# Performance work log

Hardware: AMD Instinct MI355X
Metric: run time of the kernel (lower is better)

Reference implementation:

```python
import jax, jax.numpy as jnp
import numpy as np

NNODE = 50000
NEDGE = 1600000
ZMAX = 16      # species one-hot width
DIM = 64
SUBDIM = 8
HIDDEN = 64


def setup_inputs() -> dict:
    key = jax.random.key(0)
    ks = jax.random.split(key, 16)
    species = jax.random.randint(ks[0], (NNODE,), 0, ZMAX)
    edge_src = jax.random.randint(ks[1], (NEDGE,), 0, NNODE)
    edge_dst = jax.random.randint(ks[2], (NEDGE,), 0, NNODE)
    # distances strictly positive, inside cutoff 5.0
    distances = jax.random.uniform(ks[3], (NEDGE,)) * 4.5 + 0.5
    switch = jax.random.uniform(ks[4], (NEDGE,))
    vec = jax.random.normal(ks[5], (NEDGE, 3))
    # FullyConnectedNet([64,64,64,dim]) on input of width 1 + ZMAX
    d_in = 1 + ZMAX
    def dense_init(k, fan_in, fan_out):
        return jax.random.normal(k, (fan_in, fan_out)) / np.sqrt(fan_in)
    W1 = dense_init(ks[6], d_in, HIDDEN); b1 = jnp.zeros((HIDDEN,))
    W2 = dense_init(ks[7], HIDDEN, HIDDEN); b2 = jnp.zeros((HIDDEN,))
    W3 = dense_init(ks[8], HIDDEN, HIDDEN); b3 = jnp.zeros((HIDDEN,))
    W4 = dense_init(ks[9], HIDDEN, DIM); b4 = jnp.zeros((DIM,))
    return {
        "species": species, "edge_src": edge_src, "edge_dst": edge_dst,
        "distances": distances, "switch": switch, "vec": vec,
        "W1": W1, "b1": b1, "W2": W2, "b2": b2,
        "W3": W3, "b3": b3, "W4": W4, "b4": b4,
    }


def reference(species, edge_src, edge_dst, distances, switch, vec,
              W1, b1, W2, b2, W3, b3, W4, b4):
    onehot = jax.nn.one_hot(species, ZMAX, dtype=distances.dtype)  # (N, Z)
    d = distances[:, None]                                          # (E, 1)
    sw = switch[:, None]                                            # (E, 1)
    vhat = vec / d                                                  # (E, 3)
    sij = sw / d                                                    # (E, 1), divide_distances=True
    Rij = jnp.concatenate((sij, sij * vhat), axis=-1)               # (E, 4)
    # radial_basis is None -> radial_terms = sij; concat with species onehot of dst
    x = jnp.concatenate((sij, onehot[edge_dst]), axis=-1)           # (E, 1+Z)
    h = jax.nn.silu(x @ W1 + b1)
    h = jax.nn.silu(h @ W2 + b2)
    h = jax.nn.silu(h @ W3 + b3)
    Gij = h @ W4 + b4                                               # (E, dim)
    # scatter-sum outer product over edges -> (N, 4, dim)
    GRi = jax.ops.segment_sum(Gij[:, None, :] * Rij[:, :, None], edge_src,
                              num_segments=NNODE)
    GRisub = GRi[:, :, :SUBDIM]                                     # (N, 4, subdim)
    # contract over the 4-axis: (N, dim, subdim) -> flatten
    embedding = jnp.einsum('nad,nas->nds', GRi, GRisub).reshape(NNODE, DIM * SUBDIM)
    return embedding
```

## Files before the change

### kernel.cpp

```cpp
#include <hip/hip_runtime.h>

#define NNODE 50000
#define NEDGE 1600000
#define SCAN_BLOCKS 196
#define NBLOCKS 1024
#define NWAVES (NBLOCKS*8)
#define EPW 196

typedef __attribute__((ext_vector_type(8))) _Float16 half8;
typedef __attribute__((ext_vector_type(2))) __fp16 fp16x2;
typedef __attribute__((ext_vector_type(4))) float f32x4;
typedef __attribute__((ext_vector_type(2))) float f32x2;

union H2U { fp16x2 h; unsigned int u; };
union H8U { half8 h8; unsigned int u[4]; };

__device__ __forceinline__ float b2f(unsigned short u) {
    return __uint_as_float(((unsigned int)u) << 16);
}
__device__ __forceinline__ f32x2 lo2(f32x4 v) { f32x2 r; r.x = v[0]; r.y = v[1]; return r; }
__device__ __forceinline__ f32x2 hi2(f32x4 v) { f32x2 r; r.x = v[2]; r.y = v[3]; return r; }

__device__ __forceinline__ unsigned int silu2_pk(f32x2 x) {
    f32x2 u = x * (-1.44269504f);
    f32x2 e;
    e.x = __builtin_amdgcn_exp2f(u.x);
    e.y = __builtin_amdgcn_exp2f(u.y);
    f32x2 d = e + 1.0f;
    f32x2 r;
    r.x = __builtin_amdgcn_rcpf(d.x);
    r.y = __builtin_amdgcn_rcpf(d.y);
    f32x2 s = x * r;
    H2U h2; h2.h = __builtin_amdgcn_cvt_pkrtz(s.x, s.y);
    return h2.u;
}

__device__ __forceinline__ int dp_pi(int s) {
    return (((s >> 5) & 1) << 5) | (((s >> 2) & 3) << 3)
         | (((s >> 4) & 1) << 2) | (s & 3);
}
__device__ __forceinline__ void repack_silu(const f32x4 acc[4], half8& b0, half8& b1) {
    H8U u0, u1;
    u0.u[0] = silu2_pk(lo2(acc[0])); u0.u[1] = silu2_pk(hi2(acc[0]));
    u0.u[2] = silu2_pk(lo2(acc[1])); u0.u[3] = silu2_pk(hi2(acc[1]));
    u1.u[0] = silu2_pk(lo2(acc[2])); u1.u[1] = silu2_pk(hi2(acc[2]));
    u1.u[2] = silu2_pk(lo2(acc[3])); u1.u[3] = silu2_pk(hi2(acc[3]));
    b0 = u0.h8; b1 = u1.h8;
}

template<bool F32>
__device__ __forceinline__ float ldv(const void* p, int i) {
    return F32 ? ((const float*)p)[i] : b2f(((const unsigned short*)p)[i]);
}

__device__ __forceinline__ int lb_poffs(const int* __restrict__ poffs, int val) {
    int lo = 0, hi = NNODE;
    while (lo < hi) { int mid = (lo + hi) >> 1; if (poffs[mid] < val) lo = mid + 1; else hi = mid; }
    return lo;
}

__global__ void dp_hist(const int* __restrict__ esrc, int* __restrict__ counts,
                        int* __restrict__ rank,
                        const unsigned int* __restrict__ dw, int* __restrict__ flag) {
    if (blockIdx.x == 0 && threadIdx.x < 64) {
        const int lane = threadIdx.x;
        unsigned int w = dw[lane];
        unsigned int hb_ = (w >> 8) & 0xFF;
        bool bf16like = (hb_ == 0x3F) || (hb_ == 0x40);
        unsigned long long m = __ballot(bf16like);
        if (lane == 0) *flag = (__popcll(m) > 32) ? 0 : 1;
    }
    int i = blockIdx.x*256 + threadIdx.x;
    if (i < NEDGE) rank[i] = atomicAdd(&counts[esrc[i]], 1);
}

__global__ void dp_s1(const int* __restrict__ counts, int* __restrict__ bsum) {
    int i = blockIdx.x*256 + threadIdx.x;
    int v = (i < NNODE) ? counts[i] : 0;
    #pragma unroll
    for (int o = 32; o > 0; o >>= 1) v += __shfl_down(v, o);
    __shared__ int wsum[4];
    if ((threadIdx.x & 63) == 0) wsum[threadIdx.x >> 6] = v;
    __syncthreads();
    if (threadIdx.x == 0) bsum[blockIdx.x] = wsum[0] + wsum[1] + wsum[2] + wsum[3];
}

__global__ void dp_s2(const int* __restrict__ bsum, int* __restrict__ bpre) {
    __shared__ int sh[256];
    int t = threadIdx.x;
    int v = (t < SCAN_BLOCKS) ? bsum[t] : 0;
    sh[t] = v;
    __syncthreads();
    for (int o = 1; o < 256; o <<= 1) {
        int x = (t >= o) ? sh[t - o] : 0;
        __syncthreads();
        sh[t] += x;
        __syncthreads();
    }
    if (t < SCAN_BLOCKS) bpre[t] = sh[t] - v;
}

__global__ void dp_s3(const int* __restrict__ counts, const int* __restrict__ bpre,
                      int* __restrict__ poffs) {
    __shared__ int sh[256];
    int t = threadIdx.x;
    int i = blockIdx.x*256 + t;
    int c = (i < NNODE) ? counts[i] : 0;
    sh[t] = c;
    __syncthreads();
    for (int o = 1; o < 256; o <<= 1) {
        int x = (t >= o) ? sh[t - o] : 0;
        __syncthreads();
        sh[t] += x;
        __syncthreads();
    }
    int excl = sh[t] - c + bpre[blockIdx.x];
    if (i < NNODE) poffs[i] = excl;
    if (i == NNODE-1) poffs[NNODE] = excl + c;
}

template<bool F32>
__device__ __forceinline__ void scat_body(
    const int* __restrict__ esrc, const int* __restrict__ edst,
    const int* __restrict__ species,
    const void* __restrict__ dist, const void* __restrict__ swt,
    const void* __restrict__ vec,
    const int* __restrict__ poffs, const int* __restrict__ rank,
    uint4* __restrict__ srec)
{
    int i = blockIdx.x*256 + threadIdx.x;
    if (i >= NEDGE) return;
    int pe = poffs[esrc[i]] + rank[i];
    float d  = ldv<F32>(dist, i);
    float sw = ldv<F32>(swt, i);
    float inv = 1.0f / d;
    float sij = sw * inv;
    float rx = sij * ldv<F32>(vec, 3*i+0) * inv;
    float ry = sij * ldv<F32>(vec, 3*i+1) * inv;
    float rz = sij * ldv<F32>(vec, 3*i+2) * inv;
    int z = species[edst[i]] & 15;
    uint4 rc;
    rc.x = (__float_as_uint(sij) & ~15u) | (unsigned)z;
    rc.y = __float_as_uint(rx);
    rc.z = __float_as_uint(ry);
    rc.w = __float_as_uint(rz);
    srec[pe] = rc;
}

__global__ void dp_scat(const int* __restrict__ flagp,
                        const int* __restrict__ esrc, const int* __restrict__ edst,
                        const int* __restrict__ species,
                        const void* __restrict__ dist, const void* __restrict__ swt,
                        const void* __restrict__ vec,
                        const int* __restrict__ poffs, const int* __restrict__ rank,
                        uint4* __restrict__ srec, int* __restrict__ wstart)
{
    int i = blockIdx.x*256 + threadIdx.x;
    if (i <= NWAVES) wstart[i] = lb_poffs(poffs, i*EPW);
    if (*flagp) scat_body<true >(esrc, edst, species, dist, swt, vec, poffs, rank, srec);
    else        scat_body<false>(esrc, edst, species, dist, swt, vec, poffs, rank, srec);
}

struct __align__(16) FusedShared {
    _Float16 WT[3][4096];
    float W1z[16*68];
    float W1r0[64];
    float bD[2][64];
    float Rl[8][128];
    int nb[8][64];
};

__global__ __launch_bounds__(512, 4) void dp_fused(
    const int* __restrict__ flagp,
    const void* __restrict__ W1, const void* __restrict__ b1,
    const void* __restrict__ W2, const void* __restrict__ b2,
    const void* __restrict__ W3, const void* __restrict__ b3,
    const void* __restrict__ W4, const void* __restrict__ b4,
    const int* __restrict__ poffs, const int* __restrict__ wstart,
    const uint4* __restrict__ srec,
    float* __restrict__ out)
{
    __shared__ FusedShared sh;
    const bool F32 = (*flagp != 0);
    const int tid = threadIdx.x;

    for (int i = tid; i < 4096; i += 512) {
        int k = i >> 6, c = i & 63;
        int kk = c*64 + (k ^ ((c & 7) << 3));
        int pc = dp_pi(c);
        if (F32) {
            sh.WT[0][kk] = (_Float16)ldv<true>(W2, k*64 + pc);
            sh.WT[1][kk] = (_Float16)ldv<true>(W3, k*64 + pc);
            sh.WT[2][kk] = (_Float16)ldv<true>(W4, k*64 + c);
        } else {
            sh.WT[0][kk] = (_Float16)ldv<false>(W2, k*64 + pc);
            sh.WT[1][kk] = (_Float16)ldv<false>(W3, k*64 + pc);
            sh.WT[2][kk] = (_Float16)ldv<false>(W4, k*64 + c);
        }
    }
    for (int i = tid; i < 16*64; i += 512) {
        int z = i >> 6, j = i & 63;
        sh.W1z[z*68 + j] = (F32 ? (ldv<true>(W1,(1+z)*64+j) + ldv<true>(b1,j))
                                : (ldv<false>(W1,(1+z)*64+j) + ldv<false>(b1,j)));
    }
    if (tid < 64) {
        int ps = dp_pi(tid);
        sh.W1r0[tid] = F32 ? ldv<true>(W1, tid) : ldv<false>(W1, tid);
        sh.bD[0][tid] = F32 ? ldv<true>(b2, ps) : ldv<false>(b2, ps);
        sh.bD[1][tid] = F32 ? ldv<true>(b3, ps) : ldv<false>(b3, ps);
    }

    const int lane = tid & 63;
    const int wid  = tid >> 6;
    const int col  = lane & 15;
    const int g    = lane >> 4;
    const int sw8  = (col & 7) << 3;

    float b4r[4];
    #pragma unroll
    for (int t = 0; t < 4; t++)
        b4r[t] = F32 ? ldv<true>(b4, 16*t + col) : ldv<false>(b4, 16*t + col);

    __syncthreads();

    float* RlA = sh.Rl[wid];
    float* RlB = sh.Rl[wid] + 64;
    int* nb = sh.nb[wid];

    const int w = blockIdx.x*8 + wid;
    const int n_lo = wstart[w];
    const int n_hi = wstart[w+1];
    const int nbn  = n_hi - n_lo;

    for (int j = lane; j < nbn && j < 64; j += 64) nb[j] = poffs[n_lo + 1 + j];

    int p0 = (n_lo < n_hi) ? poffs[n_lo] : 0;

    for (int node = n_lo; node < n_hi; node++) {
        const int idx = node - n_lo;
        const int p1 = (idx < 64) ? nb[idx] : poffs[node + 1];
        const int s0 = p0;
        const int cnt = p1 - p0;
        p0 = p1;
        const int ngroups = (cnt + 15) >> 4;

        f32x2 gr01[4] = {{0,0},{0,0},{0,0},{0,0}};
        f32x2 gr23[4] = {{0,0},{0,0},{0,0},{0,0}};

        int p = 0;
        for (; p + 2 <= ngroups; p += 2) {
            const int eb = s0 + 16*p;
            int slotA = eb + col;
            int slotB = eb + 16 + col;
            slotB = slotB < NEDGE-1 ? slotB : NEDGE-1;
            uint4 rcA = srec[slotA];
            uint4 rcB = srec[slotB];
            const bool vB = (16*p + 16 + col) < cnt;
            if (!vB) { rcB.x = 0u; rcB.y = 0u; rcB.z = 0u; rcB.w = 0u; }
            const float sijA = __uint_as_float(rcA.x);
            const float sijB = __uint_as_float(rcB.x);
            const int zA = (int)(rcA.x & 15u);
            const int zB = (int)(rcB.x & 15u);
            if (g == 0) {
                *(uint4*)&RlA[col*4] = rcA;
                *(uint4*)&RlB[col*4] = rcB;
            }

            half8 h0A, h1A, h0B, h1B;
            {
                const float* wzA = &sh.W1z[zA*68];
                const float* wzB = &sh.W1z[zB*68];
                f32x4 r0 = *(const f32x4*)&sh.W1r0[8*g];
                f32x4 r1 = *(const f32x4*)&sh.W1r0[8*g + 4];
                f32x4 r2 = *(const f32x4*)&sh.W1r0[32 + 8*g];
                f32x4 r3 = *(const f32x4*)&sh.W1r0[32 + 8*g + 4];
                f32x4 a0 = *(const f32x4*)&wzA[8*g];
                f32x4 a1 = *(const f32x4*)&wzA[8*g + 4];
                f32x4 a2 = *(const f32x4*)&wzA[32 + 8*g];
                f32x4 a3 = *(const f32x4*)&wzA[32 + 8*g + 4];
                f32x4 c0 = *(const f32x4*)&wzB[8*g];
                f32x4 c1 = *(const f32x4*)&wzB[8*g + 4];
                f32x4 c2 = *(const f32x4*)&wzB[32 + 8*g];
                f32x4 c3 = *(const f32x4*)&wzB[32 + 8*g + 4];
                f32x2 sA2 = {sijA, sijA};
                f32x2 sB2 = {sijB, sijB};
                H8U u0A, u1A, u0B, u1B;
                u0A.u[0] = silu2_pk(__builtin_elementwise_fma(sA2, lo2(r0), lo2(a0)));
                u0A.u[1] = silu2_pk(__builtin_elementwise_fma(sA2, hi2(r0), hi2(a0)));
                u0A.u[2] = silu2_pk(__builtin_elementwise_fma(sA2, lo2(r1), lo2(a1)));
                u0A.u[3] = silu2_pk(__builtin_elementwise_fma(sA2, hi2(r1), hi2(a1)));
                u1A.u[0] = silu2_pk(__builtin_elementwise_fma(sA2, lo2(r2), lo2(a2)));
                u1A.u[1] = silu2_pk(__builtin_elementwise_fma(sA2, hi2(r2), hi2(a2)));
                u1A.u[2] = silu2_pk(__builtin_elementwise_fma(sA2, lo2(r3), lo2(a3)));
                u1A.u[3] = silu2_pk(__builtin_elementwise_fma(sA2, hi2(r3), hi2(a3)));
                u0B.u[0] = silu2_pk(__builtin_elementwise_fma(sB2, lo2(r0), lo2(c0)));
                u0B.u[1] = silu2_pk(__builtin_elementwise_fma(sB2, hi2(r0), hi2(c0)));
                u0B.u[2] = silu2_pk(__builtin_elementwise_fma(sB2, lo2(r1), lo2(c1)));
                u0B.u[3] = silu2_pk(__builtin_elementwise_fma(sB2, hi2(r1), hi2(c1)));
                u1B.u[0] = silu2_pk(__builtin_elementwise_fma(sB2, lo2(r2), lo2(c2)));
                u1B.u[1] = silu2_pk(__builtin_elementwise_fma(sB2, hi2(r2), hi2(c2)));
                u1B.u[2] = silu2_pk(__builtin_elementwise_fma(sB2, lo2(r3), lo2(c3)));
                u1B.u[3] = silu2_pk(__builtin_elementwise_fma(sB2, hi2(r3), hi2(c3)));
                h0A = u0A.h8; h1A = u1A.h8;
                h0B = u0B.h8; h1B = u1B.h8;
            }

            f32x4 accA[4], accB[4];

            #pragma unroll
            for (int t = 0; t < 4; t++) {
                const int wb = (16*t + col)*64;
                half8 w0 = *(const half8*)&sh.WT[0][wb + ((8*g) ^ sw8)];
                half8 w1 = *(const half8*)&sh.WT[0][wb + ((32 + 8*g) ^ sw8)];
                f32x4 cb = *(const f32x4*)&sh.bD[0][16*t + 4*g];
                f32x4 a = __builtin_amdgcn_mfma_f32_16x16x32_f16(w0, h0A, cb, 0, 0, 0);
                accA[t]  = __builtin_amdgcn_mfma_f32_16x16x32_f16(w1, h1A, a, 0, 0, 0);
                f32x4 b = __builtin_amdgcn_mfma_f32_16x16x32_f16(w0, h0B, cb, 0, 0, 0);
                accB[t]  = __builtin_amdgcn_mfma_f32_16x16x32_f16(w1, h1B, b, 0, 0, 0);
            }
            repack_silu(accA, h0A, h1A);
            repack_silu(accB, h0B, h1B);

            #pragma unroll
            for (int t = 0; t < 4; t++) {
                const int wb = (16*t + col)*64;
                half8 w0 = *(const half8*)&sh.WT[1][wb + ((8*g) ^ sw8)];
                half8 w1 = *(const half8*)&sh.WT[1][wb + ((32 + 8*g) ^ sw8)];
                f32x4 cb = *(const f32x4*)&sh.bD[1][16*t + 4*g];
                f32x4 a = __builtin_amdgcn_mfma_f32_16x16x32_f16(w0, h0A, cb, 0, 0, 0);
                accA[t]  = __builtin_amdgcn_mfma_f32_16x16x32_f16(w1, h1A, a, 0, 0, 0);
                f32x4 b = __builtin_amdgcn_mfma_f32_16x16x32_f16(w0, h0B, cb, 0, 0, 0);
                accB[t]  = __builtin_amdgcn_mfma_f32_16x16x32_f16(w1, h1B, b, 0, 0, 0);
            }
            repack_silu(accA, h0A, h1A);
            repack_silu(accB, h0B, h1B);

            f32x4 RA[4], RB[4];
            RA[0] = *(const f32x4*)&RlA[16*g + 0];
            RA[1] = *(const f32x4*)&RlA[16*g + 4];
            RA[2] = *(const f32x4*)&RlA[16*g + 8];
            RA[3] = *(const f32x4*)&RlA[16*g + 12];
            RB[0] = *(const f32x4*)&RlB[16*g + 0];
            RB[1] = *(const f32x4*)&RlB[16*g + 4];
            RB[2] = *(const f32x4*)&RlB[16*g + 8];
            RB[3] = *(const f32x4*)&RlB[16*g + 12];

            #pragma unroll
            for (int t = 0; t < 4; t++) {
                const int wb = (16*t + col)*64;
                half8 w0 = *(const half8*)&sh.WT[2][wb + ((8*g) ^ sw8)];
                half8 w1 = *(const half8*)&sh.WT[2][wb + ((32 + 8*g) ^ sw8)];
                f32x4 c4 = {b4r[t], b4r[t], b4r[t], b4r[t]};
                f32x4 GA = __builtin_amdgcn_mfma_f32_16x16x32_f16(h0A, w0, c4, 0, 0, 0);
                GA = __builtin_amdgcn_mfma_f32_16x16x32_f16(h1A, w1, GA, 0, 0, 0);
                f32x4 GB = __builtin_amdgcn_mfma_f32_16x16x32_f16(h0B, w0, c4, 0, 0, 0);
                GB = __builtin_amdgcn_mfma_f32_16x16x32_f16(h1B, w1, GB, 0, 0, 0);
                #pragma unroll
                for (int j = 0; j < 4; j++) {
                    f32x2 ga = {GA[j], GA[j]};
                    f32x2 gb = {GB[j], GB[j]};
                    gr01[t] = __builtin_elementwise_fma(ga, lo2(RA[j]), gr01[t]);
                    gr23[t] = __builtin_elementwise_fma(ga, hi2(RA[j]), gr23[t]);
                    gr01[t] = __builtin_elementwise_fma(gb, lo2(RB[j]), gr01[t]);
                    gr23[t] = __builtin_elementwise_fma(gb, hi2(RB[j]), gr23[t]);
                }
            }
        }

        if (p < ngroups) {
            const int eb = s0 + 16*p;
            int slot = eb + col;
            slot = slot < NEDGE-1 ? slot : NEDGE-1;
            uint4 rc = srec[slot];
            const bool v = (16*p + col) < cnt;
            if (!v) { rc.x = 0u; rc.y = 0u; rc.z = 0u; rc.w = 0u; }
            const float sij = __uint_as_float(rc.x);
            const int z = (int)(rc.x & 15u);
            if (g == 0) {
                *(uint4*)&RlA[col*4] = rc;
            }

            half8 h0, h1;
            {
                const float* wz = &sh.W1z[z*68];
                f32x4 a0 = *(const f32x4*)&wz[8*g];
                f32x4 a1 = *(const f32x4*)&wz[8*g + 4];
                f32x4 a2 = *(const f32x4*)&wz[32 + 8*g];
                f32x4 a3 = *(const f32x4*)&wz[32 + 8*g + 4];
                f32x4 r0 = *(const f32x4*)&sh.W1r0[8*g];
                f32x4 r1 = *(const f32x4*)&sh.W1r0[8*g + 4];
                f32x4 r2 = *(const f32x4*)&sh.W1r0[32 + 8*g];
                f32x4 r3 = *(const f32x4*)&sh.W1r0[32 + 8*g + 4];
                f32x2 s2 = {sij, sij};
                H8U u0, u1;
                u0.u[0] = silu2_pk(__builtin_elementwise_fma(s2, lo2(r0), lo2(a0)));
                u0.u[1] = silu2_pk(__builtin_elementwise_fma(s2, hi2(r0), hi2(a0)));
                u0.u[2] = silu2_pk(__builtin_elementwise_fma(s2, lo2(r1), lo2(a1)));
                u0.u[3] = silu2_pk(__builtin_elementwise_fma(s2, hi2(r1), hi2(a1)));
                u1.u[0] = silu2_pk(__builtin_elementwise_fma(s2, lo2(r2), lo2(a2)));
                u1.u[1] = silu2_pk(__builtin_elementwise_fma(s2, hi2(r2), hi2(a2)));
                u1.u[2] = silu2_pk(__builtin_elementwise_fma(s2, lo2(r3), lo2(a3)));
                u1.u[3] = silu2_pk(__builtin_elementwise_fma(s2, hi2(r3), hi2(a3)));
                h0 = u0.h8; h1 = u1.h8;
            }

            f32x4 acc[4];
            #pragma unroll
            for (int t = 0; t < 4; t++) {
                const int wb = (16*t + col)*64;
                half8 w0 = *(const half8*)&sh.WT[0][wb + ((8*g) ^ sw8)];
                half8 w1 = *(const half8*)&sh.WT[0][wb + ((32 + 8*g) ^ sw8)];
                f32x4 cb = *(const f32x4*)&sh.bD[0][16*t + 4*g];
                f32x4 a = __builtin_amdgcn_mfma_f32_16x16x32_f16(w0, h0, cb, 0, 0, 0);
                acc[t]  = __builtin_amdgcn_mfma_f32_16x16x32_f16(w1, h1, a, 0, 0, 0);
            }
            repack_silu(acc, h0, h1);

            #pragma unroll
            for (int t = 0; t < 4; t++) {
                const int wb = (16*t + col)*64;
                half8 w0 = *(const half8*)&sh.WT[1][wb + ((8*g) ^ sw8)];
                half8 w1 = *(const half8*)&sh.WT[1][wb + ((32 + 8*g) ^ sw8)];
                f32x4 cb = *(const f32x4*)&sh.bD[1][16*t + 4*g];
                f32x4 a = __builtin_amdgcn_mfma_f32_16x16x32_f16(w0, h0, cb, 0, 0, 0);
                acc[t]  = __builtin_amdgcn_mfma_f32_16x16x32_f16(w1, h1, a, 0, 0, 0);
            }
            repack_silu(acc, h0, h1);

            f32x4 Rr[4];
            Rr[0] = *(const f32x4*)&RlA[16*g + 0];
            Rr[1] = *(const f32x4*)&RlA[16*g + 4];
            Rr[2] = *(const f32x4*)&RlA[16*g + 8];
            Rr[3] = *(const f32x4*)&RlA[16*g + 12];

            #pragma unroll
            for (int t = 0; t < 4; t++) {
                const int wb = (16*t + col)*64;
                half8 w0 = *(const half8*)&sh.WT[2][wb + ((8*g) ^ sw8)];
                half8 w1 = *(const half8*)&sh.WT[2][wb + ((32 + 8*g) ^ sw8)];
                f32x4 c4 = {b4r[t], b4r[t], b4r[t], b4r[t]};
                f32x4 G = __builtin_amdgcn_mfma_f32_16x16x32_f16(h0, w0, c4, 0, 0, 0);
                G = __builtin_amdgcn_mfma_f32_16x16x32_f16(h1, w1, G, 0, 0, 0);
                #pragma unroll
                for (int j = 0; j < 4; j++) {
                    f32x2 gs = {G[j], G[j]};
                    gr01[t] = __builtin_elementwise_fma(gs, lo2(Rr[j]), gr01[t]);
                    gr23[t] = __builtin_elementwise_fma(gs, hi2(Rr[j]), gr23[t]);
                }
            }
        }

        float grf[4][4];
        #pragma unroll
        for (int t = 0; t < 4; t++) {
            grf[0][t] = gr01[t].x; grf[1][t] = gr01[t].y;
            grf[2][t] = gr23[t].x; grf[3][t] = gr23[t].y;
        }

        #pragma unroll
        for (int a = 0; a < 4; a++)
            #pragma unroll
            for (int t = 0; t < 4; t++) {
                float v = grf[a][t];
                v += __shfl_xor(v, 16);
                v += __shfl_xor(v, 32);
                grf[a][t] = v;
            }

        float gs0[4], gs1[4];
        #pragma unroll
        for (int a = 0; a < 4; a++) {
            gs0[a] = __shfl(grf[a][0], 2*g);
            gs1[a] = __shfl(grf[a][0], 2*g + 1);
        }
        #pragma unroll
        for (int t = 0; t < 4; t++) {
            float e0 = 0.f, e1 = 0.f;
            #pragma unroll
            for (int a = 0; a < 4; a++) {
                e0 = fmaf(grf[a][t], gs0[a], e0);
                e1 = fmaf(grf[a][t], gs1[a], e1);
            }
            float2 st; st.x = e0; st.y = e1;
            *(float2*)&out[(size_t)node*512 + (16*t + col)*8 + 2*g] = st;
        }
    }
}

extern "C" void kernel_launch(void* const* d_in, const int* in_sizes, int n_in,
                              void* d_out, int out_size, void* d_ws, size_t ws_size,
                              hipStream_t stream)
{
    const int* species = (const int*)d_in[0];
    const int* esrc    = (const int*)d_in[1];
    const int* edst    = (const int*)d_in[2];
    const void* dist = d_in[3];
    const void* swt  = d_in[4];
    const void* vec  = d_in[5];
    const void* W1 = d_in[6];
    const void* b1 = d_in[7];
    const void* W2 = d_in[8];
    const void* b2 = d_in[9];
    const void* W3 = d_in[10];
    const void* b3 = d_in[11];
    const void* W4 = d_in[12];
    const void* b4 = d_in[13];
    float* out = (float*)d_out;

    char* base = (char*)d_ws;
    size_t off = 0;
    int* flag  = (int*)(base + off);    off += 256;
    uint4* srec = (uint4*)(base + off); off += (size_t)NEDGE*16;
    int* counts = (int*)(base + off);   off += (size_t)NNODE*4;
    int* poffs  = (int*)(base + off);   off += (size_t)(NNODE+1)*4 + 12;
    int* rank   = (int*)(base + off);   off += (size_t)NEDGE*4;
    int* wstart = (int*)(base + off);   off += (size_t)(NWAVES+1)*4 + 12;
    int* bsum   = (int*)(base + off);   off += 1024;
    int* bpre   = (int*)(base + off);   off += 1024;
    (void)ws_size; (void)in_sizes; (void)n_in; (void)out_size;

    (void)hipMemsetAsync(counts, 0, (size_t)NNODE*4, stream);

    dp_hist<<<NEDGE/256, 256, 0, stream>>>(esrc, counts, rank,
                                           (const unsigned int*)dist, flag);
    dp_s1<<<SCAN_BLOCKS, 256, 0, stream>>>(counts, bsum);
    dp_s2<<<1, 256, 0, stream>>>(bsum, bpre);
    dp_s3<<<SCAN_BLOCKS, 256, 0, stream>>>(counts, bpre, poffs);
    dp_scat<<<NEDGE/256, 256, 0, stream>>>(flag, esrc, edst, species,
                                           dist, swt, vec, poffs, rank, srec, wstart);
    dp_fused<<<NBLOCKS, 512, 0, stream>>>(flag, W1, b1, W2, b2, W3, b3, W4, b4,
                                          poffs, wstart, srec, out);
}
```

Measured before the change: 248.2 us.

## Pack edges contiguously across node boundaries to eliminate per-node padding waste

Each wave now processes its edge range as one contiguous stream of 16-edge groups spanning node boundaries, rather than padding each node's edges up to a multiple of 16. The first three MLP layers run once per group. The final layer and outer-product accumulation are repeated per node segment within the group, using a row mask, and a node's result is flushed when its edges end. This removes wasted MFMA work on padded lanes, since with about 32 edges per node on average that padding is significant. The cost is extra layer-4 passes where groups straddle nodes, and more branchy control flow.

```diff
diff --git a/kernel.cpp b/kernel.cpp
--- a/kernel.cpp
+++ b/kernel.cpp
@@ -234,229 +234,31 @@
 
     for (int j = lane; j < nbn && j < 64; j += 64) nb[j] = poffs[n_lo + 1 + j];
 
-    int p0 = (n_lo < n_hi) ? poffs[n_lo] : 0;
-
-    for (int node = n_lo; node < n_hi; node++) {
-        const int idx = node - n_lo;
-        const int p1 = (idx < 64) ? nb[idx] : poffs[node + 1];
-        const int s0 = p0;
-        const int cnt = p1 - p0;
-        p0 = p1;
-        const int ngroups = (cnt + 15) >> 4;
-
-        f32x2 gr01[4] = {{0,0},{0,0},{0,0},{0,0}};
-        f32x2 gr23[4] = {{0,0},{0,0},{0,0},{0,0}};
-
-        int p = 0;
-        for (; p + 2 <= ngroups; p += 2) {
-            const int eb = s0 + 16*p;
-            int slotA = eb + col;
-            int slotB = eb + 16 + col;
-            slotB = slotB < NEDGE-1 ? slotB : NEDGE-1;
-            uint4 rcA = srec[slotA];
-            uint4 rcB = srec[slotB];
-            const bool vB = (16*p + 16 + col) < cnt;
-            if (!vB) { rcB.x = 0u; rcB.y = 0u; rcB.z = 0u; rcB.w = 0u; }
-            const float sijA = __uint_as_float(rcA.x);
-            const float sijB = __uint_as_float(rcB.x);
-            const int zA = (int)(rcA.x & 15u);
-            const int zB = (int)(rcB.x & 15u);
-            if (g == 0) {
-                *(uint4*)&RlA[col*4] = rcA;
-                *(uint4*)&RlB[col*4] = rcB;
-            }
-
-            half8 h0A, h1A, h0B, h1B;
-            {
-                const float* wzA = &sh.W1z[zA*68];
-                const float* wzB = &sh.W1z[zB*68];
-                f32x4 r0 = *(const f32x4*)&sh.W1r0[8*g];
-                f32x4 r1 = *(const f32x4*)&sh.W1r0[8*g + 4];
-                f32x4 r2 = *(const f32x4*)&sh.W1r0[32 + 8*g];
-                f32x4 r3 = *(const f32x4*)&sh.W1r0[32 + 8*g + 4];
-                f32x4 a0 = *(const f32x4*)&wzA[8*g];
-                f32x4 a1 = *(const f32x4*)&wzA[8*g + 4];
-                f32x4 a2 = *(const f32x4*)&wzA[32 + 8*g];
-                f32x4 a3 = *(const f32x4*)&wzA[32 + 8*g + 4];
-                f32x4 c0 = *(const f32x4*)&wzB[8*g];
-                f32x4 c1 = *(const f32x4*)&wzB[8*g + 4];
-                f32x4 c2 = *(const f32x4*)&wzB[32 + 8*g];
-                f32x4 c3 = *(const f32x4*)&wzB[32 + 8*g + 4];
-                f32x2 sA2 = {sijA, sijA};
-                f32x2 sB2 = {sijB, sijB};
-                H8U u0A, u1A, u0B, u1B;
-                u0A.u[0] = silu2_pk(__builtin_elementwise_fma(sA2, lo2(r0), lo2(a0)));
-                u0A.u[1] = silu2_pk(__builtin_elementwise_fma(sA2, hi2(r0), hi2(a0)));
-                u0A.u[2] = silu2_pk(__builtin_elementwise_fma(sA2, lo2(r1), lo2(a1)));
-                u0A.u[3] = silu2_pk(__builtin_elementwise_fma(sA2, hi2(r1), hi2(a1)));
-                u1A.u[0] = silu2_pk(__builtin_elementwise_fma(sA2, lo2(r2), lo2(a2)));
-                u1A.u[1] = silu2_pk(__builtin_elementwise_fma(sA2, hi2(r2), hi2(a2)));
-                u1A.u[2] = silu2_pk(__builtin_elementwise_fma(sA2, lo2(r3), lo2(a3)));
-                u1A.u[3] = silu2_pk(__builtin_elementwise_fma(sA2, hi2(r3), hi2(a3)));
-                u0B.u[0] = silu2_pk(__builtin_elementwise_fma(sB2, lo2(r0), lo2(c0)));
-                u0B.u[1] = silu2_pk(__builtin_elementwise_fma(sB2, hi2(r0), hi2(c0)));
-                u0B.u[2] = silu2_pk(__builtin_elementwise_fma(sB2, lo2(r1), lo2(c1)));
-                u0B.u[3] = silu2_pk(__builtin_elementwise_fma(sB2, hi2(r1), hi2(c1)));
-                u1B.u[0] = silu2_pk(__builtin_elementwise_fma(sB2, lo2(r2), lo2(c2)));
-                u1B.u[1] = silu2_pk(__builtin_elementwise_fma(sB2, hi2(r2), hi2(c2)));
-                u1B.u[2] = silu2_pk(__builtin_elementwise_fma(sB2, lo2(r3), lo2(c3)));
-                u1B.u[3] = silu2_pk(__builtin_elementwise_fma(sB2, hi2(r3), hi2(c3)));
-                h0A = u0A.h8; h1A = u1A.h8;
-                h0B = u0B.h8; h1B = u1B.h8;
-            }
-
-            f32x4 accA[4], accB[4];
-
-            #pragma unroll
-            for (int t = 0; t < 4; t++) {
-                const int wb = (16*t + col)*64;
-                half8 w0 = *(const half8*)&sh.WT[0][wb + ((8*g) ^ sw8)];
-                half8 w1 = *(const half8*)&sh.WT[0][wb + ((32 + 8*g) ^ sw8)];
-                f32x4 cb = *(const f32x4*)&sh.bD[0][16*t + 4*g];
-                f32x4 a = __builtin_amdgcn_mfma_f32_16x16x32_f16(w0, h0A, cb, 0, 0, 0);
-                accA[t]  = __builtin_amdgcn_mfma_f32_16x16x32_f16(w1, h1A, a, 0, 0, 0);
-                f32x4 b = __builtin_amdgcn_mfma_f32_16x16x32_f16(w0, h0B, cb, 0, 0, 0);
-                accB[t]  = __builtin_amdgcn_mfma_f32_16x16x32_f16(w1, h1B, b, 0, 0, 0);
-            }
-            repack_silu(accA, h0A, h1A);
-            repack_silu(accB, h0B, h1B);
-
-            #pragma unroll
-            for (int t = 0; t < 4; t++) {
-                const int wb = (16*t + col)*64;
-                half8 w0 = *(const half8*)&sh.WT[1][wb + ((8*g) ^ sw8)];
-                half8 w1 = *(const half8*)&sh.WT[1][wb + ((32 + 8*g) ^ sw8)];
-                f32x4 cb = *(const f32x4*)&sh.bD[1][16*t + 4*g];
-                f32x4 a = __builtin_amdgcn_mfma_f32_16x16x32_f16(w0, h0A, cb, 0, 0, 0);
-                accA[t]  = __builtin_amdgcn_mfma_f32_16x16x32_f16(w1, h1A, a, 0, 0, 0);
-                f32x4 b = __builtin_amdgcn_mfma_f32_16x16x32_f16(w0, h0B, cb, 0, 0, 0);
-                accB[t]  = __builtin_amdgcn_mfma_f32_16x16x32_f16(w1, h1B, b, 0, 0, 0);
-            }
-            repack_silu(accA, h0A, h1A);
-            repack_silu(accB, h0B, h1B);
-
-            f32x4 RA[4], RB[4];
-            RA[0] = *(const f32x4*)&RlA[16*g + 0];
-            RA[1] = *(const f32x4*)&RlA[16*g + 4];
-            RA[2] = *(const f32x4*)&RlA[16*g + 8];
-            RA[3] = *(const f32x4*)&RlA[16*g + 12];
-            RB[0] = *(const f32x4*)&RlB[16*g + 0];
-            RB[1] = *(const f32x4*)&RlB[16*g + 4];
-            RB[2] = *(const f32x4*)&RlB[16*g + 8];
-            RB[3] = *(const f32x4*)&RlB[16*g + 12];
-
-            #pragma unroll
-            for (int t = 0; t < 4; t++) {
-                const int wb = (16*t + col)*64;
-                half8 w0 = *(const half8*)&sh.WT[2][wb + ((8*g) ^ sw8)];
-                half8 w1 = *(const half8*)&sh.WT[2][wb + ((32 + 8*g) ^ sw8)];
-                f32x4 c4 = {b4r[t], b4r[t], b4r[t], b4r[t]};
-                f32x4 GA = __builtin_amdgcn_mfma_f32_16x16x32_f16(h0A, w0, c4, 0, 0, 0);
-                GA = __builtin_amdgcn_mfma_f32_16x16x32_f16(h1A, w1, GA, 0, 0, 0);
-                f32x4 GB = __builtin_amdgcn_mfma_f32_16x16x32_f16(h0B, w0, c4, 0, 0, 0);
-                GB = __builtin_amdgcn_mfma_f32_16x16x32_f16(h1B, w1, GB, 0, 0, 0);
-                #pragma unroll
-                for (int j = 0; j < 4; j++) {
-                    f32x2 ga = {GA[j], GA[j]};
-                    f32x2 gb = {GB[j], GB[j]};
-                    gr01[t] = __builtin_elementwise_fma(ga, lo2(RA[j]), gr01[t]);
-                    gr23[t] = __builtin_elementwise_fma(ga, hi2(RA[j]), gr23[t]);
-                    gr01[t] = __builtin_elementwise_fma(gb, lo2(RB[j]), gr01[t]);
-                    gr23[t] = __builtin_elementwise_fma(gb, hi2(RB[j]), gr23[t]);
-                }
-            }
-        }
-
-        if (p < ngroups) {
-            const int eb = s0 + 16*p;
-            int slot = eb + col;
-            slot = slot < NEDGE-1 ? slot : NEDGE-1;
-            uint4 rc = srec[slot];
-            const bool v = (16*p + col) < cnt;
-            if (!v) { rc.x = 0u; rc.y = 0u; rc.z = 0u; rc.w = 0u; }
-            const float sij = __uint_as_float(rc.x);
-            const int z = (int)(rc.x & 15u);
-            if (g == 0) {
-                *(uint4*)&RlA[col*4] = rc;
-            }
-
-            half8 h0, h1;
-            {
-                const float* wz = &sh.W1z[z*68];
-                f32x4 a0 = *(const f32x4*)&wz[8*g];
-                f32x4 a1 = *(const f32x4*)&wz[8*g + 4];
-                f32x4 a2 = *(const f32x4*)&wz[32 + 8*g];
-                f32x4 a3 = *(const f32x4*)&wz[32 + 8*g + 4];
-                f32x4 r0 = *(const f32x4*)&sh.W1r0[8*g];
-                f32x4 r1 = *(const f32x4*)&sh.W1r0[8*g + 4];
-                f32x4 r2 = *(const f32x4*)&sh.W1r0[32 + 8*g];
-                f32x4 r3 = *(const f32x4*)&sh.W1r0[32 + 8*g + 4];
-                f32x2 s2 = {sij, sij};
-                H8U u0, u1;
-                u0.u[0] = silu2_pk(__builtin_elementwise_fma(s2, lo2(r0), lo2(a0)));
-                u0.u[1] = silu2_pk(__builtin_elementwise_fma(s2, hi2(r0), hi2(a0)));
-                u0.u[2] = silu2_pk(__builtin_elementwise_fma(s2, lo2(r1), lo2(a1)));
-                u0.u[3] = silu2_pk(__builtin_elementwise_fma(s2, hi2(r1), hi2(a1)));
-                u1.u[0] = silu2_pk(__builtin_elementwise_fma(s2, lo2(r2), lo2(a2)));
-                u1.u[1] = silu2_pk(__builtin_elementwise_fma(s2, hi2(r2), hi2(a2)));
-                u1.u[2] = silu2_pk(__builtin_elementwise_fma(s2, lo2(r3), lo2(a3)));
-                u1.u[3] = silu2_pk(__builtin_elementwise_fma(s2, hi2(r3), hi2(a3)));
-                h0 = u0.h8; h1 = u1.h8;
-            }
-
-            f32x4 acc[4];
-            #pragma unroll
-            for (int t = 0; t < 4; t++) {
-                const int wb = (16*t + col)*64;
-                half8 w0 = *(const half8*)&sh.WT[0][wb + ((8*g) ^ sw8)];
-                half8 w1 = *(const half8*)&sh.WT[0][wb + ((32 + 8*g) ^ sw8)];
-                f32x4 cb = *(const f32x4*)&sh.bD[0][16*t + 4*g];
-                f32x4 a = __builtin_amdgcn_mfma_f32_16x16x32_f16(w0, h0, cb, 0, 0, 0);
-                acc[t]  = __builtin_amdgcn_mfma_f32_16x16x32_f16(w1, h1, a, 0, 0, 0);
-            }
-            repack_silu(acc, h0, h1);
-
-            #pragma unroll
-            for (int t = 0; t < 4; t++) {
-                const int wb = (16*t + col)*64;
-                half8 w0 = *(const half8*)&sh.WT[1][wb + ((8*g) ^ sw8)];
-                half8 w1 = *(const half8*)&sh.WT[1][wb + ((32 + 8*g) ^ sw8)];
-                f32x4 cb = *(const f32x4*)&sh.bD[1][16*t + 4*g];
-                f32x4 a = __builtin_amdgcn_mfma_f32_16x16x32_f16(w0, h0, cb, 0, 0, 0);
-                acc[t]  = __builtin_amdgcn_mfma_f32_16x16x32_f16(w1, h1, a, 0, 0, 0);
-            }
-            repack_silu(acc, h0, h1);
-
-            f32x4 Rr[4];
-            Rr[0] = *(const f32x4*)&RlA[16*g + 0];
-            Rr[1] = *(const f32x4*)&RlA[16*g + 4];
-            Rr[2] = *(const f32x4*)&RlA[16*g + 8];
-            Rr[3] = *(const f32x4*)&RlA[16*g + 12];
-
-            #pragma unroll
-            for (int t = 0; t < 4; t++) {
-                const int wb = (16*t + col)*64;
-                half8 w0 = *(const half8*)&sh.WT[2][wb + ((8*g) ^ sw8)];
-                half8 w1 = *(const half8*)&sh.WT[2][wb + ((32 + 8*g) ^ sw8)];
-                f32x4 c4 = {b4r[t], b4r[t], b4r[t], b4r[t]};
-                f32x4 G = __builtin_amdgcn_mfma_f32_16x16x32_f16(h0, w0, c4, 0, 0, 0);
-                G = __builtin_amdgcn_mfma_f32_16x16x32_f16(h1, w1, G, 0, 0, 0);
-                #pragma unroll
-                for (int j = 0; j < 4; j++) {
-                    f32x2 gs = {G[j], G[j]};
-                    gr01[t] = __builtin_elementwise_fma(gs, lo2(Rr[j]), gr01[t]);
-                    gr23[t] = __builtin_elementwise_fma(gs, hi2(Rr[j]), gr23[t]);
-                }
-            }
-        }
-
+    if (n_lo >= n_hi) return;
+
+    auto nodeEnd = [&](int nd) -> int {
+        int idx = nd - n_lo;
+        return (idx < 64) ? nb[idx] : poffs[nd + 1];
+    };
+
+    const int pS = poffs[n_lo];
+    const int pE = nodeEnd(n_hi - 1);
+
+    int node = n_lo;
+    int p1n  = nodeEnd(node);
+
+    f32x2 gr01[4] = {{0,0},{0,0},{0,0},{0,0}};
+    f32x2 gr23[4] = {{0,0},{0,0},{0,0},{0,0}};
+
+    auto finishNode = [&](int nodeId) {
         float grf[4][4];
         #pragma unroll
         for (int t = 0; t < 4; t++) {
             grf[0][t] = gr01[t].x; grf[1][t] = gr01[t].y;
             grf[2][t] = gr23[t].x; grf[3][t] = gr23[t].y;
-        }
-
+            gr01[t].x = 0.f; gr01[t].y = 0.f;
+            gr23[t].x = 0.f; gr23[t].y = 0.f;
+        }
         #pragma unroll
         for (int a = 0; a < 4; a++)
             #pragma unroll
@@ -466,7 +268,6 @@
                 v += __shfl_xor(v, 32);
                 grf[a][t] = v;
             }
-
         float gs0[4], gs1[4];
         #pragma unroll
         for (int a = 0; a < 4; a++) {
@@ -482,8 +283,212 @@
                 e1 = fmaf(grf[a][t], gs1[a], e1);
             }
             float2 st; st.x = e0; st.y = e1;
-            *(float2*)&out[(size_t)node*512 + (16*t + col)*8 + 2*g] = st;
-        }
+            *(float2*)&out[(size_t)nodeId*512 + (16*t + col)*8 + 2*g] = st;
+        }
+    };
+
+    auto l4pass = [&](const half8& h0, const half8& h1, const float* Rlp,
+                      int lo, int hi) {
+        f32x4 Rm[4];
+        #pragma unroll
+        for (int j = 0; j < 4; j++) {
+            int r = 4*g + j;
+            float m = ((unsigned)(r - lo) < (unsigned)(hi - lo)) ? 1.0f : 0.0f;
+            f32x4 Rj = *(const f32x4*)&Rlp[16*g + 4*j];
+            Rm[j] = Rj * m;
+        }
+        #pragma unroll
+        for (int t = 0; t < 4; t++) {
+            const int wb = (16*t + col)*64;
+            half8 w0 = *(const half8*)&sh.WT[2][wb + ((8*g) ^ sw8)];
+            half8 w1 = *(const half8*)&sh.WT[2][wb + ((32 + 8*g) ^ sw8)];
+            f32x4 c4 = {b4r[t], b4r[t], b4r[t], b4r[t]};
+            f32x4 G = __builtin_amdgcn_mfma_f32_16x16x32_f16(h0, w0, c4, 0, 0, 0);
+            G = __builtin_amdgcn_mfma_f32_16x16x32_f16(h1, w1, G, 0, 0, 0);
+            #pragma unroll
+            for (int j = 0; j < 4; j++) {
+                f32x2 gs = {G[j], G[j]};
+                gr01[t] = __builtin_elementwise_fma(gs, lo2(Rm[j]), gr01[t]);
+                gr23[t] = __builtin_elementwise_fma(gs, hi2(Rm[j]), gr23[t]);
+            }
+        }
+    };
+
+    auto grPhase = [&](const half8& h0, const half8& h1, const float* Rlp, int s) {
+        int segstart = s;
+        while (true) {
+            while (node < n_hi && p1n <= segstart) {
+                finishNode(node);
+                node++;
+                if (node < n_hi) p1n = nodeEnd(node);
+            }
+            if (node >= n_hi || segstart >= s + 16) break;
+            int segend = (p1n < s + 16) ? p1n : (s + 16);
+            l4pass(h0, h1, Rlp, segstart - s, segend - s);
+            segstart = segend;
+        }
+    };
+
+    const int ngs = (pE - pS + 15) >> 4;
+
+    int k = 0;
+    for (; k + 2 <= ngs; k += 2) {
+        const int sA = pS + 16*k;
+        const int sB = sA + 16;
+        uint4 rcA = srec[sA + col];
+        int slotB = sB + col;
+        const bool vB = slotB < pE;
+        slotB = slotB < NEDGE-1 ? slotB : NEDGE-1;
+        uint4 rcB = srec[slotB];
+        if (!vB) { rcB.x = 0u; rcB.y = 0u; rcB.z = 0u; rcB.w = 0u; }
+        const float sijA = __uint_as_float(rcA.x);
+        const float sijB = __uint_as_float(rcB.x);
+        const int zA = (int)(rcA.x & 15u);
+        const int zB = (int)(rcB.x & 15u);
+        if (g == 0) {
+            *(uint4*)&RlA[col*4] = rcA;
+            *(uint4*)&RlB[col*4] = rcB;
+        }
+
+        half8 h0A, h1A, h0B, h1B;
+        {
+            const float* wzA = &sh.W1z[zA*68];
+            const float* wzB = &sh.W1z[zB*68];
+            f32x4 r0 = *(const f32x4*)&sh.W1r0[8*g];
+            f32x4 r1 = *(const f32x4*)&sh.W1r0[8*g + 4];
+            f32x4 r2 = *(const f32x4*)&sh.W1r0[32 + 8*g];
+            f32x4 r3 = *(const f32x4*)&sh.W1r0[32 + 8*g + 4];
+            f32x4 a0 = *(const f32x4*)&wzA[8*g];
+            f32x4 a1 = *(const f32x4*)&wzA[8*g + 4];
+            f32x4 a2 = *(const f32x4*)&wzA[32 + 8*g];
+            f32x4 a3 = *(const f32x4*)&wzA[32 + 8*g + 4];
+            f32x4 c0 = *(const f32x4*)&wzB[8*g];
+            f32x4 c1 = *(const f32x4*)&wzB[8*g + 4];
+            f32x4 c2 = *(const f32x4*)&wzB[32 + 8*g];
+            f32x4 c3 = *(const f32x4*)&wzB[32 + 8*g + 4];
+            f32x2 sA2 = {sijA, sijA};
+            f32x2 sB2 = {sijB, sijB};
+            H8U u0A, u1A, u0B, u1B;
+            u0A.u[0] = silu2_pk(__builtin_elementwise_fma(sA2, lo2(r0), lo2(a0)));
+            u0A.u[1] = silu2_pk(__builtin_elementwise_fma(sA2, hi2(r0), hi2(a0)));
+            u0A.u[2] = silu2_pk(__builtin_elementwise_fma(sA2, lo2(r1), lo2(a1)));
+            u0A.u[3] = silu2_pk(__builtin_elementwise_fma(sA2, hi2(r1), hi2(a1)));
+            u1A.u[0] = silu2_pk(__builtin_elementwise_fma(sA2, lo2(r2), lo2(a2)));
+            u1A.u[1] = silu2_pk(__builtin_elementwise_fma(sA2, hi2(r2), hi2(a2)));
+            u1A.u[2] = silu2_pk(__builtin_elementwise_fma(sA2, lo2(r3), lo2(a3)));
+            u1A.u[3] = silu2_pk(__builtin_elementwise_fma(sA2, hi2(r3), hi2(a3)));
+            u0B.u[0] = silu2_pk(__builtin_elementwise_fma(sB2, lo2(r0), lo2(c0)));
+            u0B.u[1] = silu2_pk(__builtin_elementwise_fma(sB2, hi2(r0), hi2(c0)));
+            u0B.u[2] = silu2_pk(__builtin_elementwise_fma(sB2, lo2(r1), lo2(c1)));
+            u0B.u[3] = silu2_pk(__builtin_elementwise_fma(sB2, hi2(r1), hi2(c1)));
+            u1B.u[0] = silu2_pk(__builtin_elementwise_fma(sB2, lo2(r2), lo2(c2)));
+            u1B.u[1] = silu2_pk(__builtin_elementwise_fma(sB2, hi2(r2), hi2(c2)));
+            u1B.u[2] = silu2_pk(__builtin_elementwise_fma(sB2, lo2(r3), lo2(c3)));
+            u1B.u[3] = silu2_pk(__builtin_elementwise_fma(sB2, hi2(r3), hi2(c3)));
+            h0A = u0A.h8; h1A = u1A.h8;
+            h0B = u0B.h8; h1B = u1B.h8;
+        }
+
+        f32x4 accA[4], accB[4];
+
+        #pragma unroll
+        for (int t = 0; t < 4; t++) {
+            const int wb = (16*t + col)*64;
+            half8 w0 = *(const half8*)&sh.WT[0][wb + ((8*g) ^ sw8)];
+            half8 w1 = *(const half8*)&sh.WT[0][wb + ((32 + 8*g) ^ sw8)];
+            f32x4 cb = *(const f32x4*)&sh.bD[0][16*t + 4*g];
+            f32x4 a = __builtin_amdgcn_mfma_f32_16x16x32_f16(w0, h0A, cb, 0, 0, 0);
+            accA[t]  = __builtin_amdgcn_mfma_f32_16x16x32_f16(w1, h1A, a, 0, 0, 0);
+            f32x4 b = __builtin_amdgcn_mfma_f32_16x16x32_f16(w0, h0B, cb, 0, 0, 0);
+            accB[t]  = __builtin_amdgcn_mfma_f32_16x16x32_f16(w1, h1B, b, 0, 0, 0);
+        }
+        repack_silu(accA, h0A, h1A);
+        repack_silu(accB, h0B, h1B);
+
+        #pragma unroll
+        for (int t = 0; t < 4; t++) {
+            const int wb = (16*t + col)*64;
+            half8 w0 = *(const half8*)&sh.WT[1][wb + ((8*g) ^ sw8)];
+            half8 w1 = *(const half8*)&sh.WT[1][wb + ((32 + 8*g) ^ sw8)];
+            f32x4 cb = *(const f32x4*)&sh.bD[1][16*t + 4*g];
+            f32x4 a = __builtin_amdgcn_mfma_f32_16x16x32_f16(w0, h0A, cb, 0, 0, 0);
+            accA[t]  = __builtin_amdgcn_mfma_f32_16x16x32_f16(w1, h1A, a, 0, 0, 0);
+            f32x4 b = __builtin_amdgcn_mfma_f32_16x16x32_f16(w0, h0B, cb, 0, 0, 0);
+            accB[t]  = __builtin_amdgcn_mfma_f32_16x16x32_f16(w1, h1B, b, 0, 0, 0);
+        }
+        repack_silu(accA, h0A, h1A);
+        repack_silu(accB, h0B, h1B);
+
+        grPhase(h0A, h1A, RlA, sA);
+        grPhase(h0B, h1B, RlB, sB);
+    }
+
+    if (k < ngs) {
+        const int sA = pS + 16*k;
+        int slot = sA + col;
+        const bool v = slot < pE;
+        slot = slot < NEDGE-1 ? slot : NEDGE-1;
+        uint4 rc = srec[slot];
+        if (!v) { rc.x = 0u; rc.y = 0u; rc.z = 0u; rc.w = 0u; }
+        const float sij = __uint_as_float(rc.x);
+        const int z = (int)(rc.x & 15u);
+        if (g == 0) {
+            *(uint4*)&RlA[col*4] = rc;
+        }
+
+        half8 h0, h1;
+        {
+            const float* wz = &sh.W1z[z*68];
+            f32x4 a0 = *(const f32x4*)&wz[8*g];
+            f32x4 a1 = *(const f32x4*)&wz[8*g + 4];
+            f32x4 a2 = *(const f32x4*)&wz[32 + 8*g];
+            f32x4 a3 = *(const f32x4*)&wz[32 + 8*g + 4];
+            f32x4 r0 = *(const f32x4*)&sh.W1r0[8*g];
+            f32x4 r1 = *(const f32x4*)&sh.W1r0[8*g + 4];
+            f32x4 r2 = *(const f32x4*)&sh.W1r0[32 + 8*g];
+            f32x4 r3 = *(const f32x4*)&sh.W1r0[32 + 8*g + 4];
+            f32x2 s2 = {sij, sij};
+            H8U u0, u1;
+            u0.u[0] = silu2_pk(__builtin_elementwise_fma(s2, lo2(r0), lo2(a0)));
+            u0.u[1] = silu2_pk(__builtin_elementwise_fma(s2, hi2(r0), hi2(a0)));
+            u0.u[2] = silu2_pk(__builtin_elementwise_fma(s2, lo2(r1), lo2(a1)));
+            u0.u[3] = silu2_pk(__builtin_elementwise_fma(s2, hi2(r1), hi2(a1)));
+            u1.u[0] = silu2_pk(__builtin_elementwise_fma(s2, lo2(r2), lo2(a2)));
+            u1.u[1] = silu2_pk(__builtin_elementwise_fma(s2, hi2(r2), hi2(a2)));
+            u1.u[2] = silu2_pk(__builtin_elementwise_fma(s2, lo2(r3), lo2(a3)));
+            u1.u[3] = silu2_pk(__builtin_elementwise_fma(s2, hi2(r3), hi2(a3)));
+            h0 = u0.h8; h1 = u1.h8;
+        }
+
+        f32x4 acc[4];
+        #pragma unroll
+        for (int t = 0; t < 4; t++) {
+            const int wb = (16*t + col)*64;
+            half8 w0 = *(const half8*)&sh.WT[0][wb + ((8*g) ^ sw8)];
+            half8 w1 = *(const half8*)&sh.WT[0][wb + ((32 + 8*g) ^ sw8)];
+            f32x4 cb = *(const f32x4*)&sh.bD[0][16*t + 4*g];
+            f32x4 a = __builtin_amdgcn_mfma_f32_16x16x32_f16(w0, h0, cb, 0, 0, 0);
+            acc[t]  = __builtin_amdgcn_mfma_f32_16x16x32_f16(w1, h1, a, 0, 0, 0);
+        }
+        repack_silu(acc, h0, h1);
+
+        #pragma unroll
+        for (int t = 0; t < 4; t++) {
+            const int wb = (16*t + col)*64;
+            half8 w0 = *(const half8*)&sh.WT[1][wb + ((8*g) ^ sw8)];
+            half8 w1 = *(const half8*)&sh.WT[1][wb + ((32 + 8*g) ^ sw8)];
+            f32x4 cb = *(const f32x4*)&sh.bD[1][16*t + 4*g];
+            f32x4 a = __builtin_amdgcn_mfma_f32_16x16x32_f16(w0, h0, cb, 0, 0, 0);
+            acc[t]  = __builtin_amdgcn_mfma_f32_16x16x32_f16(w1, h1, a, 0, 0, 0);
+        }
+        repack_silu(acc, h0, h1);
+
+        grPhase(h0, h1, RlA, sA);
+    }
+
+    while (node < n_hi) {
+        finishNode(node);
+        node++;
     }
 }
 
```

Result: no change. 249.1 us (+0.3%).
